# Kernel tuning notes

Hardware: AMD Instinct MI355X
Metric: run time of the kernel (lower is better)

Reference implementation:

```python
import jax, jax.numpy as jnp
import numpy as np

NUM_HEADS = 16
HIDDEN = 1024
HEAD_DIM = HIDDEN // NUM_HEADS
B, S, D = 2, 2048, 1024


def setup_inputs() -> dict:
    key = jax.random.key(0)
    ks = jax.random.split(key, 7)
    scale = 1.0 / np.sqrt(D)
    return {
        "query": jax.random.normal(ks[0], (B, S, D), dtype=jnp.float32),
        "key": jax.random.normal(ks[1], (B, S, D), dtype=jnp.float32),
        "value": jax.random.normal(ks[2], (B, S, D), dtype=jnp.float32),
        "Wk_w": jax.random.normal(ks[3], (HIDDEN, D), dtype=jnp.float32) * scale,
        "Wk_b": jax.random.normal(ks[4], (HIDDEN,), dtype=jnp.float32) * scale,
        "Wv_w": jax.random.normal(ks[5], (HIDDEN, D), dtype=jnp.float32) * scale,
        "Wv_b": jax.random.normal(ks[6], (HIDDEN,), dtype=jnp.float32) * scale,
    }


def reference(query, key, value, Wk_w, Wk_b, Wv_w, Wv_b):
    # NOTE: in the original torch module, self.W_v is assigned twice, so the
    # SAME Linear (Wv) projects both key and value; Wk projects query.
    b, s, _ = query.shape

    def split_heads(x):  # [b,s,hidden] -> [b,h,s,hd]
        return x.reshape(b, s, NUM_HEADS, HEAD_DIM).transpose(0, 2, 1, 3)

    q = split_heads(query @ Wk_w.T + Wk_b)
    k = split_heads(key @ Wv_w.T + Wv_b)
    v = split_heads(value @ Wv_w.T + Wv_b)

    scores = jnp.einsum("bhqd,bhkd->bhqk", q, k) / jnp.sqrt(
        jnp.asarray(HEAD_DIM, dtype=q.dtype))
    probs = jax.nn.softmax(scores, axis=-1)
    out = jnp.einsum("bhqk,bhkd->bhqd", probs, v)
    return out.transpose(0, 2, 1, 3).reshape(b, s, NUM_HEADS * HEAD_DIM)
```

## Files before the change

kernel.cpp:

```cpp
#include <hip/hip_runtime.h>
#include <stdint.h>

typedef unsigned short u16;
typedef uint32_t u32;
typedef __bf16 bf16x8 __attribute__((ext_vector_type(8)));
typedef float f32x4 __attribute__((ext_vector_type(4)));
typedef float f32x16 __attribute__((ext_vector_type(16)));
typedef u16 u16x4 __attribute__((ext_vector_type(4)));
typedef u16 u16x8 __attribute__((ext_vector_type(8)));

#define XQ_OFF 0ul
#define XK_OFF 4194304ul
#define XV_OFF 8388608ul
#define WK_OFF 12582912ul
#define WV_OFF 13631488ul
#define Q_OFF  14680064ul
#define K_OFF  18874368ul
#define V_OFF  23068672ul

#define SCQ 0.18033688011112042f

#if __has_builtin(__builtin_amdgcn_exp2f)
#define EXP2F(x) __builtin_amdgcn_exp2f(x)
#else
#define EXP2F(x) exp2f(x)
#endif

__device__ __forceinline__ u16 f2bf(float f) {
  u32 u = __float_as_uint(f);
  u32 r = (u + 0x7fffu + ((u >> 16) & 1u)) >> 16;
  return (u16)r;
}

__device__ __forceinline__ u32 pk2(float a, float b) {
  typedef __bf16 bf2_t __attribute__((ext_vector_type(2)));
  typedef float f2_t __attribute__((ext_vector_type(2)));
  f2_t v; v[0] = a; v[1] = b;
  bf2_t h = __builtin_convertvector(v, bf2_t);
  union { bf2_t h; u32 u; } cv; cv.h = h; return cv.u;
}

__device__ __forceinline__ void load_lds16(const void* g, void* l) {
  __builtin_amdgcn_global_load_lds(
      (const __attribute__((address_space(1))) u32*)g,
      (__attribute__((address_space(3))) u32*)l, 16, 0, 0);
}

__global__ __launch_bounds__(256) void cvt_tile_kernel(
    const float* __restrict__ xq, const float* __restrict__ xk,
    const float* __restrict__ xv, const float* __restrict__ wk,
    const float* __restrict__ wv, u16* __restrict__ ws) {
  __shared__ u16 tile[4096];
  const int bid = blockIdx.x;
  const float* src; size_t dstbase; int rt, ktp;
  if (bid < 3072) {
    int m = bid >> 10, loc = bid & 1023;
    src = (m == 0) ? xq : (m == 1) ? xk : xv;
    dstbase = (size_t)m * 4194304ul;
    rt = loc >> 4; ktp = loc & 15;
  } else {
    int r2 = bid - 3072;
    int m = r2 >> 8, loc = r2 & 255;
    src = m ? wv : wk;
    dstbase = WK_OFF + (size_t)m * 1048576ul;
    rt = loc >> 4; ktp = loc & 15;
  }
  const int t = threadIdx.x;
  const int row0 = t >> 4, c = t & 15;
  const int k = c * 4;
  const float* s = src + (size_t)(rt * 64 + row0) * 1024ul + ktp * 64 + k;
#pragma unroll
  for (int i = 0; i < 4; ++i) {
    float4 v = *(const float4*)(s + (size_t)i * 16384ul);
    int row = row0 + i * 16;
    u32* p = (u32*)(tile + ((k >> 5) * 2048 + ((k >> 3) & 3) * 512 + row * 8 + (k & 7)));
    p[0] = pk2(v.x, v.y);
    p[1] = pk2(v.z, v.w);
  }
  __syncthreads();
  u16* dst = ws + dstbase + (size_t)(rt * 32 + ktp * 2) * 2048ul;
#pragma unroll
  for (int so = 0; so < 4096; so += 2048)
    *(u16x8*)(dst + so + t * 8) = *(const u16x8*)(tile + so + t * 8);
}

__global__ __launch_bounds__(256, 3) void proj_kernel(u16* __restrict__ ws,
                                                      const float* __restrict__ bk,
                                                      const float* __restrict__ bv) {
  const int proj = blockIdx.z;
  const int mtile = blockIdx.x;
  const int ntile = blockIdx.y;
  const u16* A = ws + (size_t)proj * 4194304ul;
  const u16* Bw = ws + ((proj == 0) ? WK_OFF : WV_OFF);
  const float* bias = (proj == 0) ? bk : bv;
  u16* outQ = ws + Q_OFF;
  u16* outK = ws + K_OFF;
  u16* outV = ws + V_OFF;

  const int t = threadIdx.x;
  const int w = t >> 6, lane = t & 63;
  const int wm = w >> 1, wn = w & 1;
  const int c32 = lane & 31, g2 = lane >> 5;

  const u16* Aw = A + (size_t)(2 * mtile + wm) * 65536ul + (size_t)g2 * 512ul + (size_t)c32 * 8ul;
  const u16* Bb = Bw + (size_t)(2 * ntile + wn) * 65536ul + (size_t)g2 * 512ul + (size_t)c32 * 8ul;

  f32x16 acc[2][2];
#pragma unroll
  for (int rf = 0; rf < 2; ++rf)
#pragma unroll
    for (int cf = 0; cf < 2; ++cf)
#pragma unroll
      for (int i = 0; i < 16; ++i) acc[rf][cf][i] = 0.f;

  bf16x8 ab[4][2], bb[4][2];
#pragma unroll
  for (int s = 0; s < 4; ++s)
#pragma unroll
    for (int f = 0; f < 2; ++f) {
      ab[s][f] = *(const bf16x8*)(Aw + (size_t)s * 1024ul + f * 256);
      bb[s][f] = *(const bf16x8*)(Bb + (size_t)s * 1024ul + f * 256);
    }

#pragma unroll 1
  for (int ks = 0; ks < 60; ks += 4) {
#pragma unroll
    for (int s = 0; s < 4; ++s) {
#pragma unroll
      for (int rf = 0; rf < 2; ++rf)
#pragma unroll
        for (int cf = 0; cf < 2; ++cf)
          acc[rf][cf] =
              __builtin_amdgcn_mfma_f32_32x32x16_bf16(ab[s][rf], bb[s][cf], acc[rf][cf], 0, 0, 0);
      const size_t o = (size_t)(ks + 4 + s) * 1024ul;
#pragma unroll
      for (int f = 0; f < 2; ++f) {
        ab[s][f] = *(const bf16x8*)(Aw + o + f * 256);
        bb[s][f] = *(const bf16x8*)(Bb + o + f * 256);
      }
    }
  }
#pragma unroll
  for (int s = 0; s < 4; ++s)
#pragma unroll
    for (int rf = 0; rf < 2; ++rf)
#pragma unroll
      for (int cf = 0; cf < 2; ++cf)
        acc[rf][cf] =
            __builtin_amdgcn_mfma_f32_32x32x16_bf16(ab[s][rf], bb[s][cf], acc[rf][cf], 0, 0, 0);

  const int m0w = mtile * 128 + wm * 64, n0w = ntile * 128 + wn * 64;
#pragma unroll
  for (int cf = 0; cf < 2; ++cf) {
    const int col = n0w + cf * 32 + c32;
    const float bvv = bias[col];
    const int h = col >> 6, d = col & 63;
#pragma unroll
    for (int rf = 0; rf < 2; ++rf) {
#pragma unroll
      for (int q = 0; q < 4; ++q) {
        const int mbase = m0w + rf * 32 + q * 8 + g2 * 4;
        const int b = mbase >> 11;
        const int bh = b * 16 + h;
        if (proj == 2) {
          const int s = mbase & 2047;
          u16x4 pk;
#pragma unroll
          for (int r = 0; r < 4; ++r) pk[r] = f2bf(acc[rf][cf][q * 4 + r] + bvv);
          size_t idx = (size_t)bh * 131072ul + (size_t)(s >> 6) * 4096ul +
                       (size_t)((s & 63) >> 3) * 512ul + (size_t)d * 8ul + (size_t)(s & 7);
          *(u16x4*)(outV + idx) = pk;
        } else {
          u16* dst = (proj == 0) ? outQ : outK;
#pragma unroll
          for (int r = 0; r < 4; ++r) {
            const int m = mbase + r;
            const int s = m & 2047;
            float y = acc[rf][cf][q * 4 + r] + bvv;
            if (proj == 0) y *= SCQ;
            size_t idx;
            if (proj == 0)
              idx = (size_t)bh * 131072ul + (size_t)(s >> 7) * 8192ul + (size_t)(d >> 3) * 1024ul +
                    (size_t)(s & 127) * 8ul + (size_t)(d & 7);
            else
              idx = (size_t)bh * 131072ul + (size_t)(s >> 6) * 4096ul + (size_t)(d >> 3) * 512ul +
                    (size_t)(s & 63) * 8ul + (size_t)(d & 7);
            dst[idx] = f2bf(y);
          }
        }
      }
    }
  }
}

__global__ __launch_bounds__(256, 2) void attn_kernel(const u16* __restrict__ ws,
                                                      float* __restrict__ out) {
  const int bh = blockIdx.x, qtile = blockIdx.y;
  const int b = bh >> 4, h = bh & 15;
  const int t = threadIdx.x, w = t >> 6, lane = t & 63, g = lane >> 4, c = lane & 15;

  __shared__ __align__(16) u16 Ps[4][1280];

  const u16* Qg = ws + Q_OFF + (size_t)bh * 131072ul + (size_t)qtile * 8192ul;
  const u16* Kg = ws + K_OFF + (size_t)bh * 131072ul;
  const u16* Vg = ws + V_OFF + (size_t)bh * 131072ul;

  bf16x8 qf[2][2];
#pragma unroll
  for (int ntq = 0; ntq < 2; ++ntq)
#pragma unroll
    for (int ks = 0; ks < 2; ++ks)
      qf[ntq][ks] = *(const bf16x8*)(Qg + (ks * 4 + g) * 1024 + (w * 32 + ntq * 16 + c) * 8);

  u16x8 ou;
#pragma unroll
  for (int i = 0; i < 8; ++i) ou[i] = (u16)0x3F80;
  union { u16x8 u; bf16x8 b; } ocv; ocv.u = ou;
  const bf16x8 onesf = ocv.b;

  f32x4 O[2][4], Lacc[2];
#pragma unroll
  for (int mtq = 0; mtq < 2; ++mtq) {
    Lacc[mtq] = (f32x4){0.f, 0.f, 0.f, 0.f};
#pragma unroll
    for (int nt = 0; nt < 4; ++nt) O[mtq][nt] = (f32x4){0.f, 0.f, 0.f, 0.f};
  }

  u16* Psw = Ps[w];

  bf16x8 kf[2][4];
#pragma unroll
  for (int ks = 0; ks < 2; ++ks)
#pragma unroll
    for (int mtk = 0; mtk < 4; ++mtk)
      kf[ks][mtk] = *(const bf16x8*)(Kg + (ks * 4 + g) * 512 + (mtk * 16 + c) * 8);

#pragma unroll 1
  for (int j = 0; j < 32; ++j) {
    const u16* Vj = Vg + (size_t)j * 4096ul;
    bf16x8 vf[2][4];
#pragma unroll
    for (int ksh = 0; ksh < 2; ++ksh)
#pragma unroll
      for (int nt = 0; nt < 4; ++nt)
        vf[ksh][nt] = *(const bf16x8*)(Vj + (ksh * 4 + g) * 512 + (nt * 16 + c) * 8);

    f32x4 St[4][2];
#pragma unroll
    for (int mtk = 0; mtk < 4; ++mtk)
#pragma unroll
      for (int ntq = 0; ntq < 2; ++ntq) St[mtk][ntq] = (f32x4){0.f, 0.f, 0.f, 0.f};
#pragma unroll
    for (int ks = 0; ks < 2; ++ks)
#pragma unroll
      for (int mtk = 0; mtk < 4; ++mtk)
#pragma unroll
        for (int ntq = 0; ntq < 2; ++ntq)
          St[mtk][ntq] =
              __builtin_amdgcn_mfma_f32_16x16x32_bf16(kf[ks][mtk], qf[ntq][ks], St[mtk][ntq], 0, 0, 0);

    const u16* Kn = Kg + (size_t)((j < 31) ? (j + 1) : 31) * 4096ul;
#pragma unroll
    for (int ks = 0; ks < 2; ++ks)
#pragma unroll
      for (int mtk = 0; mtk < 4; ++mtk)
        kf[ks][mtk] = *(const bf16x8*)(Kn + (ks * 4 + g) * 512 + (mtk * 16 + c) * 8);

#pragma unroll
    for (int mtk = 0; mtk < 4; ++mtk)
#pragma unroll
      for (int ntq = 0; ntq < 2; ++ntq)
#pragma unroll
        for (int r = 0; r < 4; ++r) St[mtk][ntq][r] = EXP2F(St[mtk][ntq][r]);

#pragma unroll
    for (int ksh = 0; ksh < 2; ++ksh) {
#pragma unroll
      for (int ntq = 0; ntq < 2; ++ntq)
#pragma unroll
        for (int m2 = 0; m2 < 2; ++m2) {
          const int mtk = ksh * 2 + m2;
          u32 lo = pk2(St[mtk][ntq][0], St[mtk][ntq][1]);
          u32 hi = pk2(St[mtk][ntq][2], St[mtk][ntq][3]);
          u32* p = (u32*)(Psw + (ntq * 16 + c) * 40 + m2 * 16 + g * 4);
          p[0] = lo; p[1] = hi;
        }
      asm volatile("s_waitcnt lgkmcnt(0)" ::: "memory");
      bf16x8 pf[2];
#pragma unroll
      for (int mtq = 0; mtq < 2; ++mtq)
        pf[mtq] = *(const bf16x8*)(Psw + (mtq * 16 + c) * 40 + g * 8);
#pragma unroll
      for (int mtq = 0; mtq < 2; ++mtq) {
        Lacc[mtq] = __builtin_amdgcn_mfma_f32_16x16x32_bf16(pf[mtq], onesf, Lacc[mtq], 0, 0, 0);
#pragma unroll
        for (int nt = 0; nt < 4; ++nt)
          O[mtq][nt] =
              __builtin_amdgcn_mfma_f32_16x16x32_bf16(pf[mtq], vf[ksh][nt], O[mtq][nt], 0, 0, 0);
      }
    }
  }

  const int q0 = qtile * 128 + w * 32;
#pragma unroll
  for (int mtq = 0; mtq < 2; ++mtq)
#pragma unroll
    for (int r = 0; r < 4; ++r) {
      const float inv = 1.0f / Lacc[mtq][r];
      const int q = q0 + mtq * 16 + g * 4 + r;
      float* rowp = out + (size_t)(b * 2048 + q) * 1024ul + h * 64;
#pragma unroll
      for (int nt = 0; nt < 4; ++nt) rowp[nt * 16 + c] = O[mtq][nt][r] * inv;
    }
}

extern "C" void kernel_launch(void* const* d_in, const int* in_sizes, int n_in,
                              void* d_out, int out_size, void* d_ws, size_t ws_size,
                              hipStream_t stream) {
  const float* q = (const float*)d_in[0];
  const float* k = (const float*)d_in[1];
  const float* v = (const float*)d_in[2];
  const float* wk = (const float*)d_in[3];
  const float* bk = (const float*)d_in[4];
  const float* wv = (const float*)d_in[5];
  const float* bv = (const float*)d_in[6];
  u16* ws = (u16*)d_ws;
  float* out = (float*)d_out;

  cvt_tile_kernel<<<3584, 256, 0, stream>>>(q, k, v, wk, wv, ws);
  proj_kernel<<<dim3(32, 8, 3), 256, 0, stream>>>(ws, bk, bv);
  attn_kernel<<<dim3(32, 16), 256, 0, stream>>>(ws, out);
}
```

Measured before the change: 183.1 us.

## Double-buffer K and V tiles in registers across attention iterations

The attention loop is restructured so both K and V fragments for the next tile are prefetched into a second register set while the current tile is computed, unrolled by two with A/B buffers. Previously only K was prefetched, and V was loaded at the top of each iteration. The P staging buffer is widened so all four key subtiles are written before a single LDS wait instead of two. This hides more global-load latency but doubles the K/V register footprint, which may raise VGPR pressure under the 2-blocks launch bound.

After: 183.4 us. Within noise of the previous version (+0.1%).

```diff
diff --git a/kernel.cpp b/kernel.cpp
--- a/kernel.cpp
+++ b/kernel.cpp
@@ -193,13 +193,79 @@
   }
 }
 
+__device__ __forceinline__ void load_kv(const u16* __restrict__ Kj,
+                                        const u16* __restrict__ Vj,
+                                        bf16x8 (&kf)[2][4], bf16x8 (&vf)[2][4],
+                                        int c, int g) {
+#pragma unroll
+  for (int ks = 0; ks < 2; ++ks)
+#pragma unroll
+    for (int mtk = 0; mtk < 4; ++mtk)
+      kf[ks][mtk] = *(const bf16x8*)(Kj + (ks * 4 + g) * 512 + (mtk * 16 + c) * 8);
+#pragma unroll
+  for (int ksh = 0; ksh < 2; ++ksh)
+#pragma unroll
+    for (int nt = 0; nt < 4; ++nt)
+      vf[ksh][nt] = *(const bf16x8*)(Vj + (ksh * 4 + g) * 512 + (nt * 16 + c) * 8);
+}
+
+__device__ __forceinline__ void attn_step(const bf16x8 (&kf)[2][4], const bf16x8 (&vf)[2][4],
+                                          const bf16x8 (&qf)[2][2], const bf16x8 onesf,
+                                          f32x4 (&O)[2][4], f32x4 (&Lacc)[2],
+                                          u16* __restrict__ Psw, int c, int g) {
+  f32x4 St[4][2];
+#pragma unroll
+  for (int mtk = 0; mtk < 4; ++mtk)
+#pragma unroll
+    for (int ntq = 0; ntq < 2; ++ntq) St[mtk][ntq] = (f32x4){0.f, 0.f, 0.f, 0.f};
+#pragma unroll
+  for (int ks = 0; ks < 2; ++ks)
+#pragma unroll
+    for (int mtk = 0; mtk < 4; ++mtk)
+#pragma unroll
+      for (int ntq = 0; ntq < 2; ++ntq)
+        St[mtk][ntq] =
+            __builtin_amdgcn_mfma_f32_16x16x32_bf16(kf[ks][mtk], qf[ntq][ks], St[mtk][ntq], 0, 0, 0);
+#pragma unroll
+  for (int mtk = 0; mtk < 4; ++mtk)
+#pragma unroll
+    for (int ntq = 0; ntq < 2; ++ntq)
+#pragma unroll
+      for (int r = 0; r < 4; ++r) St[mtk][ntq][r] = EXP2F(St[mtk][ntq][r]);
+#pragma unroll
+  for (int ntq = 0; ntq < 2; ++ntq)
+#pragma unroll
+    for (int mtk = 0; mtk < 4; ++mtk) {
+      u32 lo = pk2(St[mtk][ntq][0], St[mtk][ntq][1]);
+      u32 hi = pk2(St[mtk][ntq][2], St[mtk][ntq][3]);
+      u32* p = (u32*)(Psw + (ntq * 16 + c) * 72 + mtk * 16 + g * 4);
+      p[0] = lo; p[1] = hi;
+    }
+  asm volatile("s_waitcnt lgkmcnt(0)" ::: "memory");
+#pragma unroll
+  for (int ksh = 0; ksh < 2; ++ksh) {
+    bf16x8 pf[2];
+#pragma unroll
+    for (int mtq = 0; mtq < 2; ++mtq)
+      pf[mtq] = *(const bf16x8*)(Psw + (mtq * 16 + c) * 72 + ksh * 32 + g * 8);
+#pragma unroll
+    for (int mtq = 0; mtq < 2; ++mtq) {
+      Lacc[mtq] = __builtin_amdgcn_mfma_f32_16x16x32_bf16(pf[mtq], onesf, Lacc[mtq], 0, 0, 0);
+#pragma unroll
+      for (int nt = 0; nt < 4; ++nt)
+        O[mtq][nt] =
+            __builtin_amdgcn_mfma_f32_16x16x32_bf16(pf[mtq], vf[ksh][nt], O[mtq][nt], 0, 0, 0);
+    }
+  }
+}
+
 __global__ __launch_bounds__(256, 2) void attn_kernel(const u16* __restrict__ ws,
                                                       float* __restrict__ out) {
   const int bh = blockIdx.x, qtile = blockIdx.y;
   const int b = bh >> 4, h = bh & 15;
   const int t = threadIdx.x, w = t >> 6, lane = t & 63, g = lane >> 4, c = lane & 15;
 
-  __shared__ __align__(16) u16 Ps[4][1280];
+  __shared__ __align__(16) u16 Ps[4][2304];
 
   const u16* Qg = ws + Q_OFF + (size_t)bh * 131072ul + (size_t)qtile * 8192ul;
   const u16* Kg = ws + K_OFF + (size_t)bh * 131072ul;
@@ -228,77 +294,17 @@
 
   u16* Psw = Ps[w];
 
-  bf16x8 kf[2][4];
-#pragma unroll
-  for (int ks = 0; ks < 2; ++ks)
-#pragma unroll
-    for (int mtk = 0; mtk < 4; ++mtk)
-      kf[ks][mtk] = *(const bf16x8*)(Kg + (ks * 4 + g) * 512 + (mtk * 16 + c) * 8);
+  bf16x8 kfA[2][4], vfA[2][4], kfB[2][4], vfB[2][4];
+  load_kv(Kg, Vg, kfA, vfA, c, g);
 
 #pragma unroll 1
-  for (int j = 0; j < 32; ++j) {
-    const u16* Vj = Vg + (size_t)j * 4096ul;
-    bf16x8 vf[2][4];
-#pragma unroll
-    for (int ksh = 0; ksh < 2; ++ksh)
-#pragma unroll
-      for (int nt = 0; nt < 4; ++nt)
-        vf[ksh][nt] = *(const bf16x8*)(Vj + (ksh * 4 + g) * 512 + (nt * 16 + c) * 8);
-
-    f32x4 St[4][2];
-#pragma unroll
-    for (int mtk = 0; mtk < 4; ++mtk)
-#pragma unroll
-      for (int ntq = 0; ntq < 2; ++ntq) St[mtk][ntq] = (f32x4){0.f, 0.f, 0.f, 0.f};
-#pragma unroll
-    for (int ks = 0; ks < 2; ++ks)
-#pragma unroll
-      for (int mtk = 0; mtk < 4; ++mtk)
-#pragma unroll
-        for (int ntq = 0; ntq < 2; ++ntq)
-          St[mtk][ntq] =
-              __builtin_amdgcn_mfma_f32_16x16x32_bf16(kf[ks][mtk], qf[ntq][ks], St[mtk][ntq], 0, 0, 0);
-
-    const u16* Kn = Kg + (size_t)((j < 31) ? (j + 1) : 31) * 4096ul;
-#pragma unroll
-    for (int ks = 0; ks < 2; ++ks)
-#pragma unroll
-      for (int mtk = 0; mtk < 4; ++mtk)
-        kf[ks][mtk] = *(const bf16x8*)(Kn + (ks * 4 + g) * 512 + (mtk * 16 + c) * 8);
-
-#pragma unroll
-    for (int mtk = 0; mtk < 4; ++mtk)
-#pragma unroll
-      for (int ntq = 0; ntq < 2; ++ntq)
-#pragma unroll
-        for (int r = 0; r < 4; ++r) St[mtk][ntq][r] = EXP2F(St[mtk][ntq][r]);
-
-#pragma unroll
-    for (int ksh = 0; ksh < 2; ++ksh) {
-#pragma unroll
-      for (int ntq = 0; ntq < 2; ++ntq)
-#pragma unroll
-        for (int m2 = 0; m2 < 2; ++m2) {
-          const int mtk = ksh * 2 + m2;
-          u32 lo = pk2(St[mtk][ntq][0], St[mtk][ntq][1]);
-          u32 hi = pk2(St[mtk][ntq][2], St[mtk][ntq][3]);
-          u32* p = (u32*)(Psw + (ntq * 16 + c) * 40 + m2 * 16 + g * 4);
-          p[0] = lo; p[1] = hi;
-        }
-      asm volatile("s_waitcnt lgkmcnt(0)" ::: "memory");
-      bf16x8 pf[2];
-#pragma unroll
-      for (int mtq = 0; mtq < 2; ++mtq)
-        pf[mtq] = *(const bf16x8*)(Psw + (mtq * 16 + c) * 40 + g * 8);
-#pragma unroll
-      for (int mtq = 0; mtq < 2; ++mtq) {
-        Lacc[mtq] = __builtin_amdgcn_mfma_f32_16x16x32_bf16(pf[mtq], onesf, Lacc[mtq], 0, 0, 0);
-#pragma unroll
-        for (int nt = 0; nt < 4; ++nt)
-          O[mtq][nt] =
-              __builtin_amdgcn_mfma_f32_16x16x32_bf16(pf[mtq], vf[ksh][nt], O[mtq][nt], 0, 0, 0);
-      }
-    }
+  for (int j2 = 0; j2 < 16; ++j2) {
+    const int jB = 2 * j2 + 1;
+    load_kv(Kg + (size_t)jB * 4096ul, Vg + (size_t)jB * 4096ul, kfB, vfB, c, g);
+    attn_step(kfA, vfA, qf, onesf, O, Lacc, Psw, c, g);
+    const int jn = (jB < 31) ? (jB + 1) : 31;
+    load_kv(Kg + (size_t)jn * 4096ul, Vg + (size_t)jn * 4096ul, kfA, vfA, c, g);
+    attn_step(kfB, vfB, qf, onesf, O, Lacc, Psw, c, g);
   }
 
   const int q0 = qtile * 128 + w * 32;
```
